# Performance work log

Measured on AMD Instinct MI355X. Metric: run time of the kernel, lower is better.

## Reference

```python
import jax, jax.numpy as jnp
import numpy as np

B, N, F, K = 512, 128, 128, 4


def setup_inputs() -> dict:
    key = jax.random.key(0)
    ks = jax.random.split(key, 12)
    # xavier-normal-ish scales
    s_rw = float(np.sqrt(2.0 / (F + F)))
    s_sw = float(np.sqrt(2.0 / (F + F)))
    inp = {
        "H": jax.random.normal(ks[0], (B, N, F), dtype=jnp.float32),
        "E": jax.random.uniform(ks[1], (B, N, N, K), dtype=jnp.float32),
        "RW1": jax.random.normal(ks[2], (F, F, K), dtype=jnp.float32) * s_rw,
        "SW1": jax.random.normal(ks[3], (F, F), dtype=jnp.float32) * s_sw,
        "RW2": jax.random.normal(ks[4], (F, F, K), dtype=jnp.float32) * s_rw,
        "SW2": jax.random.normal(ks[5], (F, F), dtype=jnp.float32) * s_sw,
        "RW3": jax.random.normal(ks[6], (F, F, K), dtype=jnp.float32) * s_rw,
        "SW3": jax.random.normal(ks[7], (F, F), dtype=jnp.float32) * s_sw,
        "W1": jax.random.normal(ks[8], (F, 20), dtype=jnp.float32) * float(np.sqrt(1.0 / F)),
        "b1": jnp.zeros((20,), dtype=jnp.float32),
        "W2": jax.random.normal(ks[9], (20, 1), dtype=jnp.float32) * float(np.sqrt(1.0 / 20)),
        "b2": jnp.zeros((1,), dtype=jnp.float32),
    }
    return inp


def _rgcn_conv(H, E, D, RW, SW):
    # einsum('bi,bijk,bjm,mnk->bin') done in two GEMM-shaped steps
    M = jnp.einsum('bijk,bjm->bimk', E, H)          # [B,N,F,K]
    msg = jnp.einsum('bimk,mnk->bin', M, RW)        # [B,N,F]
    return jax.nn.sigmoid(msg * D[:, :, None] + jnp.einsum('bij,jl->bil', H, SW))


def reference(H, E, RW1, SW1, RW2, SW2, RW3, SW3, W1, b1, W2, b2):
    # degree norm with self-loops: (E + eye)[b,i,:,:].sum() = E.sum((2,3)) + K
    k = jnp.asarray(E.shape[-1], dtype=E.dtype)
    D = 1.0 / (E.sum(axis=(2, 3)) + k)              # [B,N]
    H = _rgcn_conv(H, E, D, RW1, SW1)
    H = _rgcn_conv(H, E, D, RW2, SW2)
    H = _rgcn_conv(H, E, D, RW3, SW3)
    h = jnp.maximum(H @ W1 + b1, 0.1 * (H @ W1 + b1))  # LeakyReLU(0.1)
    score = jnp.mean(jax.nn.sigmoid(h @ W2 + b2))
    return score
```

## Files before the change

### kernel.cpp

```cpp
#include <hip/hip_runtime.h>
#include <math.h>

#define BB 512
#define NN 128
#define FF 128
#define KK 4
#define GS_PITCH 132

typedef __attribute__((ext_vector_type(8))) short bf16x8;
typedef __attribute__((ext_vector_type(4))) float f32x4;

__device__ inline unsigned short f2bf(float x) {
  union { float f; unsigned int u; } v; v.f = x;
  unsigned int r = v.u + 0x7fff + ((v.u >> 16) & 1);
  return (unsigned short)(r >> 16);
}
__device__ inline float bf2f(unsigned short h) {
  union { unsigned int u; float f; } v; v.u = ((unsigned int)h) << 16; return v.f;
}

__global__ __launch_bounds__(256) void k_prep(
    const float* __restrict__ E, const float* __restrict__ H,
    const float* __restrict__ RW1, const float* __restrict__ SW1,
    const float* __restrict__ RW2, const float* __restrict__ SW2,
    const float* __restrict__ RW3, const float* __restrict__ SW3,
    unsigned short* __restrict__ Eb, unsigned short* __restrict__ Ha,
    unsigned short* __restrict__ W2L, float* __restrict__ Dv,
    float* __restrict__ Sum, int* __restrict__ Cnt)
{
  const int bid = blockIdx.x;
  if (bid < 16384) {
    int wave = threadIdx.x >> 6;
    int lane = threadIdx.x & 63;
    int row  = bid * 4 + wave;
    const float* p = E + (size_t)row * 512 + lane * 8;
    f32x4 a = *(const f32x4*)p;
    f32x4 b = *(const f32x4*)(p + 4);
    float s = a[0] + a[1] + a[2] + a[3] + b[0] + b[1] + b[2] + b[3];
    #pragma unroll
    for (int off = 32; off > 0; off >>= 1) s += __shfl_down(s, off, 64);
    if (lane == 0) Dv[row] = 1.0f / (s + 4.0f);
    union { unsigned short h[8]; f32x4 v; } u;
    u.h[0] = f2bf(a[0]); u.h[1] = f2bf(a[1]); u.h[2] = f2bf(a[2]); u.h[3] = f2bf(a[3]);
    u.h[4] = f2bf(b[0]); u.h[5] = f2bf(b[1]); u.h[6] = f2bf(b[2]); u.h[7] = f2bf(b[3]);
    *(f32x4*)(Eb + (size_t)row * 512 + lane * 8) = u.v;
  } else if (bid < 20480) {
    size_t i = ((size_t)(bid - 16384) * 256 + threadIdx.x) * 8;
    f32x4 a = *(const f32x4*)(H + i);
    f32x4 b = *(const f32x4*)(H + i + 4);
    union { unsigned short h[8]; f32x4 v; } u;
    u.h[0] = f2bf(a[0]); u.h[1] = f2bf(a[1]); u.h[2] = f2bf(a[2]); u.h[3] = f2bf(a[3]);
    u.h[4] = f2bf(b[0]); u.h[5] = f2bf(b[1]); u.h[6] = f2bf(b[2]); u.h[7] = f2bf(b[3]);
    *(f32x4*)(Ha + i) = u.v;
  } else {
    int t2  = bid - 20480;
    int tab = t2 / 320;
    int idx = (t2 - tab * 320) * 256 + threadIdx.x;
    int m = idx & 127;
    int c = idx >> 7;
    const float* RW = (tab == 0) ? RW1 : (tab == 1) ? RW2 : RW3;
    const float* SW = (tab == 0) ? SW1 : (tab == 1) ? SW2 : SW3;
    float v = (c < 512) ? RW[m * 512 + c] : SW[m * 128 + (c - 512)];
    W2L[(size_t)tab * 81920 + idx] = f2bf(v);
    if (t2 == 0 && threadIdx.x == 0) { *Sum = 0.0f; *Cnt = 0; }
  }
}

__global__ __launch_bounds__(512, 1) void k_layer(
    const unsigned short* __restrict__ Eb,
    const unsigned short* __restrict__ Hin,
    const unsigned short* __restrict__ W2L,
    const float* __restrict__ Dv,
    unsigned short* __restrict__ Hout)
{
  __shared__ unsigned short Gs2[2][128 * GS_PITCH];

  const int b = blockIdx.x;
  const unsigned short* E_b = Eb  + (size_t)b * 65536;
  const unsigned short* H_b = Hin + (size_t)b * 16384;

  const int tid = threadIdx.x;
  const int w = tid >> 6, l = tid & 63;
  const int wr = w >> 1, wc = w & 1;
  const int lq = l >> 4, lm = l & 15;

  const unsigned short* E_row0 = E_b + (size_t)(wr * 32 + lm) * 512 + lq * 8;

  auto run1a = [&](int s, unsigned short* GsD) {
    f32x4 gacc[4][2] = {};
    #pragma unroll
    for (int k0 = 0; k0 < 128; k0 += 32) {
      bf16x8 fa[4], fb[2];
      #pragma unroll
      for (int f = 0; f < 4; ++f)
        fa[f] = *(const bf16x8*)(W2L + (w * 64 + f * 16 + lm) * 128 + k0 + lq * 8);
      #pragma unroll
      for (int g = 0; g < 2; ++g)
        fb[g] = *(const bf16x8*)(H_b + (s * 32 + g * 16 + lm) * 128 + k0 + lq * 8);
      #pragma unroll
      for (int f = 0; f < 4; ++f)
        #pragma unroll
        for (int g = 0; g < 2; ++g)
          gacc[f][g] = __builtin_amdgcn_mfma_f32_16x16x32_bf16(fa[f], fb[g], gacc[f][g], 0, 0, 0);
    }
    #pragma unroll
    for (int f = 0; f < 4; ++f) {
      int n = w * 16 + f * 4 + lq;
      #pragma unroll
      for (int g = 0; g < 2; ++g) {
        int jl = g * 16 + lm;
        union { unsigned short h4[4]; uint2 v; } u;
        u.h4[0] = f2bf(gacc[f][g][0]); u.h4[1] = f2bf(gacc[f][g][1]);
        u.h4[2] = f2bf(gacc[f][g][2]); u.h4[3] = f2bf(gacc[f][g][3]);
        *(uint2*)(&GsD[n * GS_PITCH + jl * 4]) = u.v;
      }
    }
  };

  f32x4 macc[2][4] = {};

  run1a(0, Gs2[0]);
  asm volatile("s_waitcnt lgkmcnt(0)\n\ts_barrier" ::: "memory");

  #pragma unroll
  for (int s = 0; s < 4; ++s) {
    bf16x8 eaR[8];
    #pragma unroll
    for (int kt = 0; kt < 4; ++kt)
      #pragma unroll
      for (int f = 0; f < 2; ++f)
        eaR[kt * 2 + f] = *(const bf16x8*)(E_row0 + (size_t)f * 16 * 512 + s * 128 + kt * 32);

    if (s < 3) run1a(s + 1, Gs2[(s + 1) & 1]);

    const unsigned short* GsR = Gs2[s & 1];
    #pragma unroll
    for (int kt = 0; kt < 4; ++kt) {
      bf16x8 fb[4];
      #pragma unroll
      for (int g = 0; g < 4; ++g)
        fb[g] = *(const bf16x8*)(&GsR[(wc * 64 + g * 16 + lm) * GS_PITCH + kt * 32 + lq * 8]);
      #pragma unroll
      for (int f = 0; f < 2; ++f)
        #pragma unroll
        for (int g = 0; g < 4; ++g)
          macc[f][g] = __builtin_amdgcn_mfma_f32_16x16x32_bf16(eaR[kt * 2 + f], fb[g], macc[f][g], 0, 0, 0);
    }

    asm volatile("s_waitcnt lgkmcnt(0)\n\ts_barrier" ::: "memory");
  }

  f32x4 sacc[2][4] = {};
  #pragma unroll
  for (int k0 = 0; k0 < 128; k0 += 32) {
    bf16x8 fa[2], fb[4];
    #pragma unroll
    for (int f = 0; f < 2; ++f)
      fa[f] = *(const bf16x8*)(H_b + (wr * 32 + f * 16 + lm) * 128 + k0 + lq * 8);
    #pragma unroll
    for (int g = 0; g < 4; ++g)
      fb[g] = *(const bf16x8*)(W2L + (512 + wc * 64 + g * 16 + lm) * 128 + k0 + lq * 8);
    #pragma unroll
    for (int f = 0; f < 2; ++f)
      #pragma unroll
      for (int g = 0; g < 4; ++g)
        sacc[f][g] = __builtin_amdgcn_mfma_f32_16x16x32_bf16(fa[f], fb[g], sacc[f][g], 0, 0, 0);
  }

  const float* dvb = Dv + b * 128;
  unsigned short* Os = (unsigned short*)Gs2[0];
  #pragma unroll
  for (int f = 0; f < 2; ++f) {
    int i0 = wr * 32 + f * 16 + lq * 4;
    f32x4 d = *(const f32x4*)(dvb + i0);
    #pragma unroll
    for (int g = 0; g < 4; ++g) {
      int n = wc * 64 + g * 16 + lm;
      #pragma unroll
      for (int r = 0; r < 4; ++r) {
        float v = fmaf(macc[f][g][r], d[r], sacc[f][g][r]);
        Os[(i0 + r) * 128 + n] = f2bf(1.0f / (1.0f + __expf(-v)));
      }
    }
  }
  __syncthreads();
  unsigned short* O_b = Hout + (size_t)b * 16384;
  {
    int off = tid * 32;
    f32x4 v0 = *(const f32x4*)(Os + off);
    f32x4 v1 = *(const f32x4*)(Os + off + 8);
    f32x4 v2 = *(const f32x4*)(Os + off + 16);
    f32x4 v3 = *(const f32x4*)(Os + off + 24);
    *(f32x4*)(O_b + off)      = v0;
    *(f32x4*)(O_b + off + 8)  = v1;
    *(f32x4*)(O_b + off + 16) = v2;
    *(f32x4*)(O_b + off + 24) = v3;
  }
}

__global__ __launch_bounds__(256) void k_mlp(
    const unsigned short* __restrict__ H,
    const float* __restrict__ W1, const float* __restrict__ b1,
    const float* __restrict__ W2, const float* __restrict__ b2,
    float* __restrict__ Sum, int* __restrict__ Cnt, float* __restrict__ out)
{
  __shared__ float W1s[128 * 20];
  __shared__ float b1s[20], W2s[20];
  __shared__ float red[256];
  for (int i = threadIdx.x; i < 2560; i += 256) W1s[i] = W1[i];
  if (threadIdx.x < 20) { b1s[threadIdx.x] = b1[threadIdx.x]; W2s[threadIdx.x] = W2[threadIdx.x]; }
  __syncthreads();

  int row = blockIdx.x * 256 + threadIdx.x;
  float h[20];
  #pragma unroll
  for (int j = 0; j < 20; ++j) h[j] = b1s[j];
  const unsigned short* hr = H + (size_t)row * 128;
  for (int m8 = 0; m8 < 128; m8 += 8) {
    f32x4 pk = *(const f32x4*)(hr + m8);
    const unsigned short* us = (const unsigned short*)&pk;
    #pragma unroll
    for (int e = 0; e < 8; ++e) {
      float x = bf2f(us[e]);
      #pragma unroll
      for (int j = 0; j < 20; ++j) h[j] = fmaf(x, W1s[(m8 + e) * 20 + j], h[j]);
    }
  }
  float v = b2[0];
  #pragma unroll
  for (int j = 0; j < 20; ++j) {
    float t = h[j];
    t = fmaxf(t, 0.1f * t);
    v = fmaf(t, W2s[j], v);
  }
  float s = 1.0f / (1.0f + __expf(-v));

  red[threadIdx.x] = s;
  __syncthreads();
  #pragma unroll
  for (int off = 128; off > 0; off >>= 1) {
    if (threadIdx.x < off) red[threadIdx.x] += red[threadIdx.x + off];
    __syncthreads();
  }
  if (threadIdx.x == 0) {
    atomicAdd(Sum, red[0]);
    __threadfence();
    int c = atomicAdd(Cnt, 1);
    if (c == gridDim.x - 1) {
      float tot = atomicAdd(Sum, 0.0f);
      out[0] = tot * (1.0f / 65536.0f);
    }
  }
}

extern "C" void kernel_launch(void* const* d_in, const int* in_sizes, int n_in,
                              void* d_out, int out_size, void* d_ws, size_t ws_size,
                              hipStream_t stream) {
  (void)in_sizes; (void)n_in; (void)out_size; (void)ws_size;
  const float* H   = (const float*)d_in[0];
  const float* E   = (const float*)d_in[1];
  const float* RW1 = (const float*)d_in[2];
  const float* SW1 = (const float*)d_in[3];
  const float* RW2 = (const float*)d_in[4];
  const float* SW2 = (const float*)d_in[5];
  const float* RW3 = (const float*)d_in[6];
  const float* SW3 = (const float*)d_in[7];
  const float* W1  = (const float*)d_in[8];
  const float* b1  = (const float*)d_in[9];
  const float* W2  = (const float*)d_in[10];
  const float* b2  = (const float*)d_in[11];
  float* out = (float*)d_out;

  char* w = (char*)d_ws;
  float*          wsD   = (float*)w;           w += (size_t)65536 * 4;
  unsigned short* wsEb  = (unsigned short*)w;  w += (size_t)33554432 * 2;
  unsigned short* wsHa  = (unsigned short*)w;  w += (size_t)8388608 * 2;
  unsigned short* wsHb  = (unsigned short*)w;  w += (size_t)8388608 * 2;
  unsigned short* wsHc  = (unsigned short*)w;  w += (size_t)8388608 * 2;
  unsigned short* wsHd  = (unsigned short*)w;  w += (size_t)8388608 * 2;
  unsigned short* wsW2  = (unsigned short*)w;  w += (size_t)3 * 81920 * 2;
  float*          wsSum = (float*)w;           w += 64;
  int*            wsCnt = (int*)w;             w += 64;

  k_prep<<<21440, 256, 0, stream>>>(E, H, RW1, SW1, RW2, SW2, RW3, SW3,
                                    wsEb, wsHa, wsW2, wsD, wsSum, wsCnt);

  k_layer<<<BB, 512, 0, stream>>>(wsEb, wsHa, wsW2,          wsD, wsHb);
  k_layer<<<BB, 512, 0, stream>>>(wsEb, wsHb, wsW2 + 81920,  wsD, wsHc);
  k_layer<<<BB, 512, 0, stream>>>(wsEb, wsHc, wsW2 + 163840, wsD, wsHd);

  k_mlp<<<BB * NN / 256, 256, 0, stream>>>(wsHd, W1, b1, W2, b2, wsSum, wsCnt, out);
}
```

Before: 527.0 us.

## Compute full G tile into shared memory before single E×G GEMM loop

Removes the double-buffered interleaving of the H×RW GEMM with the E×G GEMM. All four G slices are now computed up front into one large shared buffer (128×520 bf16), followed by a single barrier and a flat 16-step K loop over E. This drops three barriers and simplifies the schedule, but gives up the overlap of G production with E loads and MFMA consumption. The larger LDS footprint (~133 KB) is allowed only because occupancy is already one block per CU. An extra __syncthreads is added before the output buffer reuses the same LDS region.

```diff
diff --git a/kernel.cpp b/kernel.cpp
--- a/kernel.cpp
+++ b/kernel.cpp
@@ -5,7 +5,7 @@
 #define NN 128
 #define FF 128
 #define KK 4
-#define GS_PITCH 132
+#define GT_PITCH 520
 
 typedef __attribute__((ext_vector_type(8))) short bf16x8;
 typedef __attribute__((ext_vector_type(4))) float f32x4;
@@ -73,7 +73,7 @@
     const float* __restrict__ Dv,
     unsigned short* __restrict__ Hout)
 {
-  __shared__ unsigned short Gs2[2][128 * GS_PITCH];
+  __shared__ unsigned short Gs[128 * GT_PITCH];
 
   const int b = blockIdx.x;
   const unsigned short* E_b = Eb  + (size_t)b * 65536;
@@ -84,9 +84,8 @@
   const int wr = w >> 1, wc = w & 1;
   const int lq = l >> 4, lm = l & 15;
 
-  const unsigned short* E_row0 = E_b + (size_t)(wr * 32 + lm) * 512 + lq * 8;
-
-  auto run1a = [&](int s, unsigned short* GsD) {
+  #pragma unroll
+  for (int s = 0; s < 4; ++s) {
     f32x4 gacc[4][2] = {};
     #pragma unroll
     for (int k0 = 0; k0 < 128; k0 += 32) {
@@ -108,46 +107,32 @@
       int n = w * 16 + f * 4 + lq;
       #pragma unroll
       for (int g = 0; g < 2; ++g) {
-        int jl = g * 16 + lm;
+        int j = s * 32 + g * 16 + lm;
         union { unsigned short h4[4]; uint2 v; } u;
         u.h4[0] = f2bf(gacc[f][g][0]); u.h4[1] = f2bf(gacc[f][g][1]);
         u.h4[2] = f2bf(gacc[f][g][2]); u.h4[3] = f2bf(gacc[f][g][3]);
-        *(uint2*)(&GsD[n * GS_PITCH + jl * 4]) = u.v;
+        *(uint2*)(&Gs[n * GT_PITCH + j * 4]) = u.v;
       }
     }
-  };
+  }
+  asm volatile("s_waitcnt lgkmcnt(0)\n\ts_barrier" ::: "memory");
 
   f32x4 macc[2][4] = {};
-
-  run1a(0, Gs2[0]);
-  asm volatile("s_waitcnt lgkmcnt(0)\n\ts_barrier" ::: "memory");
-
-  #pragma unroll
-  for (int s = 0; s < 4; ++s) {
-    bf16x8 eaR[8];
-    #pragma unroll
-    for (int kt = 0; kt < 4; ++kt)
-      #pragma unroll
-      for (int f = 0; f < 2; ++f)
-        eaR[kt * 2 + f] = *(const bf16x8*)(E_row0 + (size_t)f * 16 * 512 + s * 128 + kt * 32);
-
-    if (s < 3) run1a(s + 1, Gs2[(s + 1) & 1]);
-
-    const unsigned short* GsR = Gs2[s & 1];
-    #pragma unroll
-    for (int kt = 0; kt < 4; ++kt) {
-      bf16x8 fb[4];
+  const unsigned short* E_row0 = E_b + (size_t)(wr * 32 + lm) * 512 + lq * 8;
+  #pragma unroll 4
+  for (int kt = 0; kt < 16; ++kt) {
+    bf16x8 ea[2], fb[4];
+    #pragma unroll
+    for (int f = 0; f < 2; ++f)
+      ea[f] = *(const bf16x8*)(E_row0 + (size_t)f * 16 * 512 + kt * 32);
+    #pragma unroll
+    for (int g = 0; g < 4; ++g)
+      fb[g] = *(const bf16x8*)(&Gs[(wc * 64 + g * 16 + lm) * GT_PITCH + kt * 32 + lq * 8]);
+    #pragma unroll
+    for (int f = 0; f < 2; ++f)
       #pragma unroll
       for (int g = 0; g < 4; ++g)
-        fb[g] = *(const bf16x8*)(&GsR[(wc * 64 + g * 16 + lm) * GS_PITCH + kt * 32 + lq * 8]);
-      #pragma unroll
-      for (int f = 0; f < 2; ++f)
-        #pragma unroll
-        for (int g = 0; g < 4; ++g)
-          macc[f][g] = __builtin_amdgcn_mfma_f32_16x16x32_bf16(eaR[kt * 2 + f], fb[g], macc[f][g], 0, 0, 0);
-    }
-
-    asm volatile("s_waitcnt lgkmcnt(0)\n\ts_barrier" ::: "memory");
+        macc[f][g] = __builtin_amdgcn_mfma_f32_16x16x32_bf16(ea[f], fb[g], macc[f][g], 0, 0, 0);
   }
 
   f32x4 sacc[2][4] = {};
@@ -168,7 +153,8 @@
   }
 
   const float* dvb = Dv + b * 128;
-  unsigned short* Os = (unsigned short*)Gs2[0];
+  __syncthreads();
+  unsigned short* Os = Gs;
   #pragma unroll
   for (int f = 0; f < 2; ++f) {
     int i0 = wr * 32 + f * 16 + lq * 4;
```

Result: faster. 502.2 us (-4.7%).
